# Optimization experiments

Measured on AMD Instinct MI355X. Metric: run time of the kernel, lower is better.

## Reference

```python
import jax, jax.numpy as jnp
import numpy as np

N, FIN = 4096, 128
HEADS = [8, 1]
FEATS = [64, 64]
NEG_SLOPE = 0.2
EDGE_P = 0.01  # edge density for the synthetic graph


def _init_w(key, shape, fan_in, fan_out):
    # VarianceScaling(1.0, 'fan_avg', 'uniform')
    limit = jnp.sqrt(3.0 / ((fan_in + fan_out) / 2.0))
    return jax.random.uniform(key, shape, jnp.float32, -limit, limit)


def setup_inputs() -> dict:
    key = jax.random.key(0)
    ks = jax.random.split(key, 12)
    x = jax.random.normal(ks[0], (N, FIN), jnp.float32)
    # additive connectivity mask: 0 on edges (incl. self-loops), -1e9 elsewhere
    adj = jax.random.bernoulli(ks[1], EDGE_P, (N, N))
    adj = adj | jnp.eye(N, dtype=bool)
    mask = jnp.where(adj, 0.0, -1e9).astype(jnp.float32)

    fin0, out0 = FIN, HEADS[0] * FEATS[0]
    fin1, out1 = out0, HEADS[1] * FEATS[1]
    W0 = _init_w(ks[2], (fin0, out0), fin0, out0)
    b0 = jnp.zeros((out0,), jnp.float32)
    a_src0 = _init_w(ks[3], (1, HEADS[0], FEATS[0]), 1, HEADS[0] * FEATS[0])
    a_tgt0 = _init_w(ks[4], (1, HEADS[0], FEATS[0]), 1, HEADS[0] * FEATS[0])
    W1 = _init_w(ks[5], (fin1, out1), fin1, out1)
    b1 = jnp.zeros((out1,), jnp.float32)
    a_src1 = _init_w(ks[6], (1, HEADS[1], FEATS[1]), 1, HEADS[1] * FEATS[1])
    a_tgt1 = _init_w(ks[7], (1, HEADS[1], FEATS[1]), 1, HEADS[1] * FEATS[1])
    return {
        "node_features": x, "connectivity_mask": mask,
        "W0": W0, "b0": b0, "a_src0": a_src0, "a_tgt0": a_tgt0,
        "W1": W1, "b1": b1, "a_src1": a_src1, "a_tgt1": a_tgt1,
    }


def _gat_layer(x, mask, W, b, a_src, a_tgt, num_heads, num_features):
    # (N, FIN) @ (FIN, H*F) -> (N, H, F)
    proj = (x @ W + b).reshape(-1, num_heads, num_features)
    s_src = jnp.sum(proj * a_src, axis=-1)  # (N, H)
    s_tgt = jnp.sum(proj * a_tgt, axis=-1)  # (N, H)
    # (H, N, 1) + (H, 1, N) -> (H, N, N)
    scores = s_src.T[:, :, None] + s_tgt.T[:, None, :]
    scores = jax.nn.leaky_relu(scores, negative_slope=NEG_SLOPE)
    att = jax.nn.softmax(scores + mask[None, :, :], axis=-1)  # (H, N, N)
    out = jnp.einsum('hnm,mhf->nhf', att, proj)  # (N, H, F)
    return out.reshape(-1, num_heads * num_features)


def reference(node_features, connectivity_mask, W0, b0, a_src0, a_tgt0,
              W1, b1, a_src1, a_tgt1):
    h = _gat_layer(node_features, connectivity_mask, W0, b0, a_src0, a_tgt0,
                   HEADS[0], FEATS[0])
    h = _gat_layer(h, connectivity_mask, W1, b1, a_src1, a_tgt1,
                   HEADS[1], FEATS[1])
    return h  # (N, HEADS[1]*FEATS[1])
```

## Files before the change

kernel.cpp:

```cpp
#include <hip/hip_runtime.h>
#include <hip/hip_bf16.h>

#define NNODES 4096
#define CAP 256


__global__ __launch_bounds__(256) void phase1_kernel(
    const float* __restrict__ mask, int* __restrict__ deg, int* __restrict__ cols,
    const float* __restrict__ x, const float* __restrict__ W0,
    const float* __restrict__ b0, const float* __restrict__ a_src0,
    const float* __restrict__ a_tgt0, float* __restrict__ proj0,
    float* __restrict__ ssrc0, float* __restrict__ stgt0) {
  __shared__ float smem[32 * 36 + 32 * 64];
  const int t = threadIdx.x;
  if (blockIdx.x >= 1024) {
    const int n = blockIdx.x - 1024;
    const int lane = t & 63, wid = t >> 6;
    int* wsum = (int*)smem;
    const float4* row = (const float4*)(mask + (size_t)n * NNODES);
    float4 v[4];
    int cnt = 0;
#pragma unroll
    for (int j = 0; j < 4; ++j) {
      v[j] = row[t + 256 * j];
      cnt += (v[j].x == 0.0f) + (v[j].y == 0.0f) + (v[j].z == 0.0f) +
             (v[j].w == 0.0f);
    }
    int xs = cnt;
#pragma unroll
    for (int o = 1; o < 64; o <<= 1) {
      int y = __shfl_up(xs, o);
      if (lane >= o) xs += y;
    }
    if (lane == 63) wsum[wid] = xs;
    __syncthreads();
    int base = 0;
    for (int w = 0; w < wid; ++w) base += wsum[w];
    int off = base + xs - cnt;
    if (t == 0) {
      int total = wsum[0] + wsum[1] + wsum[2] + wsum[3];
      deg[n] = total < CAP ? total : CAP;
    }
    int* dst = cols + (size_t)n * CAP;
#pragma unroll
    for (int j = 0; j < 4; ++j) {
      const int c0 = (t + 256 * j) * 4;
      float fv[4] = {v[j].x, v[j].y, v[j].z, v[j].w};
#pragma unroll
      for (int k = 0; k < 4; ++k) {
        if (fv[k] == 0.0f) {
          if (off < CAP) dst[off] = c0 + k;
          ++off;
        }
      }
    }
  } else {
    float(*As)[36] = (float(*)[36])smem;
    float(*Ws)[64] = (float(*)[64])(smem + 32 * 36);
    const int bx = blockIdx.x;
    const int brow = (bx & 127) * 32;
    const int head = bx >> 7;
    const int bcol = head * 64;
    const int tx = t & 15, ty = t >> 4;
    const int ar = t >> 3, ak = (t & 7) * 4;
    float acc[2][4] = {};
    for (int c = 0; c < 4; ++c) {
      const int k0 = c * 32;
      *(float4*)&As[ar][ak] =
          *(const float4*)&x[(size_t)(brow + ar) * 128 + k0 + ak];
#pragma unroll
      for (int q = 0; q < 2; ++q) {
        int i = t + q * 256;
        int k = i >> 4, c4 = (i & 15) * 4;
        *(float4*)&Ws[k][c4] =
            *(const float4*)&W0[(size_t)(k0 + k) * 512 + bcol + c4];
      }
      __syncthreads();
#pragma unroll 2
      for (int kk = 0; kk < 32; kk += 4) {
        float4 a0 = *(const float4*)&As[ty * 2 + 0][kk];
        float4 a1 = *(const float4*)&As[ty * 2 + 1][kk];
#pragma unroll
        for (int j = 0; j < 4; ++j) {
          float4 w = *(const float4*)&Ws[kk + j][tx * 4];
          float av0 = ((const float*)&a0)[j];
          float av1 = ((const float*)&a1)[j];
          acc[0][0] = fmaf(av0, w.x, acc[0][0]);
          acc[0][1] = fmaf(av0, w.y, acc[0][1]);
          acc[0][2] = fmaf(av0, w.z, acc[0][2]);
          acc[0][3] = fmaf(av0, w.w, acc[0][3]);
          acc[1][0] = fmaf(av1, w.x, acc[1][0]);
          acc[1][1] = fmaf(av1, w.y, acc[1][1]);
          acc[1][2] = fmaf(av1, w.z, acc[1][2]);
          acc[1][3] = fmaf(av1, w.w, acc[1][3]);
        }
      }
      __syncthreads();
    }
    const float4 bv = *(const float4*)&b0[bcol + tx * 4];
    const float4 as = *(const float4*)&a_src0[head * 64 + tx * 4];
    const float4 at = *(const float4*)&a_tgt0[head * 64 + tx * 4];
#pragma unroll
    for (int r = 0; r < 2; ++r) {
      float4 o;
      o.x = acc[r][0] + bv.x; o.y = acc[r][1] + bv.y;
      o.z = acc[r][2] + bv.z; o.w = acc[r][3] + bv.w;
      const size_t node = brow + ty * 2 + r;
      *(float4*)&proj0[node * 512 + bcol + tx * 4] = o;
      float ps = o.x * as.x + o.y * as.y + o.z * as.z + o.w * as.w;
      float pt = o.x * at.x + o.y * at.y + o.z * at.z + o.w * at.w;
#pragma unroll
      for (int m = 8; m; m >>= 1) {
        ps += __shfl_xor(ps, m);
        pt += __shfl_xor(pt, m);
      }
      if (tx == 0) {
        ssrc0[node * 8 + head] = ps;
        stgt0[node * 8 + head] = pt;
      }
    }
  }
}

__global__ __launch_bounds__(128) void attn8h_kernel(
    const float* __restrict__ proj0, const float* __restrict__ ssrc0,
    const float* __restrict__ stgt0, const int* __restrict__ deg,
    const int* __restrict__ cols, float* __restrict__ h0) {
  const int b = blockIdx.x;
  const int fh = (b & 7) >> 2;
  const int n = ((b >> 3) << 2) + (b & 3);
  const int t = threadIdx.x;
  const int lane = t & 63, wid = t >> 6;
  __shared__ int sm_[CAP];
  __shared__ float sw[CAP * 5];
  __shared__ float sinv[4];
  __shared__ float4 buf[64];
  const int d = deg[n];
  for (int i = t; i < d; i += 128) sm_[i] = cols[(size_t)n * CAP + i];
  __syncthreads();
  const int hbase = fh * 4;
  for (int i = t; i < d * 4; i += 128) {
    const int e = i >> 2, h = i & 3;
    float s = ssrc0[n * 8 + hbase + h] + stgt0[sm_[e] * 8 + hbase + h];
    sw[e * 5 + h] = s >= 0.f ? s : 0.2f * s;
  }
  __syncthreads();
  for (int h = wid; h < 4; h += 2) {
    float mx = -1e30f;
    for (int e = lane; e < d; e += 64) mx = fmaxf(mx, sw[e * 5 + h]);
#pragma unroll
    for (int o = 32; o; o >>= 1) mx = fmaxf(mx, __shfl_xor(mx, o));
    float sum = 0.f;
    for (int e = lane; e < d; e += 64) {
      float w = __expf(sw[e * 5 + h] - mx);
      sw[e * 5 + h] = w;
      sum += w;
    }
#pragma unroll
    for (int o = 32; o; o >>= 1) sum += __shfl_xor(sum, o);
    if (lane == 0) sinv[h] = 1.0f / sum;
  }
  __syncthreads();
  const int f4l = t & 63, grp = t >> 6;
  const int hl = f4l >> 4;
  float4 acc = make_float4(0.f, 0.f, 0.f, 0.f);
  for (int e = grp; e < d; e += 2) {
    const float w = sw[e * 5 + hl];
    const float4 pv =
        *(const float4*)&proj0[(size_t)sm_[e] * 512 + fh * 256 + f4l * 4];
    acc.x = fmaf(w, pv.x, acc.x);
    acc.y = fmaf(w, pv.y, acc.y);
    acc.z = fmaf(w, pv.z, acc.z);
    acc.w = fmaf(w, pv.w, acc.w);
  }
  if (grp == 1) buf[f4l] = acc;
  __syncthreads();
  if (grp == 0) {
    const float4 o2 = buf[f4l];
    const float s = sinv[hl];
    float4 o;
    o.x = (acc.x + o2.x) * s;
    o.y = (acc.y + o2.y) * s;
    o.z = (acc.z + o2.z) * s;
    o.w = (acc.w + o2.w) * s;
    *(float4*)&h0[(size_t)n * 512 + fh * 256 + f4l * 4] = o;
  }
}

__global__ __launch_bounds__(256) void gemm32x64_v2(
    const float* __restrict__ A, int lda, const float* __restrict__ W, int ldw,
    float* __restrict__ C, int ldc) {
  __shared__ float As[32][36];
  __shared__ float Ws[32][64];
  const int t = threadIdx.x;
  const int brow = blockIdx.x * 32;
  const int bcol = blockIdx.y * 64;
  const int k0base = blockIdx.z * 128;
  C += (size_t)blockIdx.z * gridDim.x * 32 * ldc;
  const int tx = t & 15, ty = t >> 4;
  const int ar = t >> 3, ak = (t & 7) * 4;
  float acc[2][4] = {};
  for (int c = 0; c < 4; ++c) {
    const int k0 = k0base + c * 32;
    *(float4*)&As[ar][ak] = *(const float4*)&A[(size_t)(brow + ar) * lda + k0 + ak];
#pragma unroll
    for (int q = 0; q < 2; ++q) {
      int i = t + q * 256;
      int k = i >> 4, c4 = (i & 15) * 4;
      *(float4*)&Ws[k][c4] = *(const float4*)&W[(size_t)(k0 + k) * ldw + bcol + c4];
    }
    __syncthreads();
#pragma unroll 2
    for (int kk = 0; kk < 32; kk += 4) {
      float4 a0 = *(const float4*)&As[ty * 2 + 0][kk];
      float4 a1 = *(const float4*)&As[ty * 2 + 1][kk];
#pragma unroll
      for (int j = 0; j < 4; ++j) {
        float4 w = *(const float4*)&Ws[kk + j][tx * 4];
        float av0 = ((const float*)&a0)[j];
        float av1 = ((const float*)&a1)[j];
        acc[0][0] = fmaf(av0, w.x, acc[0][0]);
        acc[0][1] = fmaf(av0, w.y, acc[0][1]);
        acc[0][2] = fmaf(av0, w.z, acc[0][2]);
        acc[0][3] = fmaf(av0, w.w, acc[0][3]);
        acc[1][0] = fmaf(av1, w.x, acc[1][0]);
        acc[1][1] = fmaf(av1, w.y, acc[1][1]);
        acc[1][2] = fmaf(av1, w.z, acc[1][2]);
        acc[1][3] = fmaf(av1, w.w, acc[1][3]);
      }
    }
    __syncthreads();
  }
#pragma unroll
  for (int r = 0; r < 2; ++r) {
    float4 o;
    o.x = acc[r][0]; o.y = acc[r][1]; o.z = acc[r][2]; o.w = acc[r][3];
    *(float4*)&C[(size_t)(brow + ty * 2 + r) * ldc + bcol + tx * 4] = o;
  }
}

__global__ __launch_bounds__(256) void reduce_scores1_kernel(
    const float* __restrict__ part, const float* __restrict__ bias,
    const float* __restrict__ a_src1, const float* __restrict__ a_tgt1,
    float* __restrict__ proj1, float* __restrict__ ssrc1,
    float* __restrict__ stgt1) {
  const int i = blockIdx.x * 256 + threadIdx.x;
  const float4* p = (const float4*)part;
  float4 a = p[i], b = p[i + 65536], c = p[i + 131072], d = p[i + 196608];
  const int f4 = i & 15;
  const float4 bb = *(const float4*)&bias[f4 * 4];
  float4 r;
  r.x = a.x + b.x + c.x + d.x + bb.x;
  r.y = a.y + b.y + c.y + d.y + bb.y;
  r.z = a.z + b.z + c.z + d.z + bb.z;
  r.w = a.w + b.w + c.w + d.w + bb.w;
  ((float4*)proj1)[i] = r;
  const float4 as = *(const float4*)&a_src1[f4 * 4];
  const float4 at = *(const float4*)&a_tgt1[f4 * 4];
  float ps = r.x * as.x + r.y * as.y + r.z * as.z + r.w * as.w;
  float pt = r.x * at.x + r.y * at.y + r.z * at.z + r.w * at.w;
#pragma unroll
  for (int m = 8; m; m >>= 1) {
    ps += __shfl_xor(ps, m);
    pt += __shfl_xor(pt, m);
  }
  if (f4 == 0) {
    const int node = i >> 4;
    ssrc1[node] = ps;
    stgt1[node] = pt;
  }
}

__global__ void attn1_kernel(
    const float* __restrict__ proj, const float* __restrict__ s_src,
    const float* __restrict__ s_tgt, const int* __restrict__ deg,
    const int* __restrict__ cols, float* __restrict__ out) {
  const int n = blockIdx.x;
  const int tid = threadIdx.x;
  __shared__ int sm_[CAP];
  __shared__ float sw[CAP];
  const int d = deg[n];
  for (int i = tid; i < d; i += 64) sm_[i] = cols[(size_t)n * CAP + i];
  __syncthreads();
  const float ssn = s_src[n];
  for (int i = tid; i < d; i += 64) {
    float s = ssn + s_tgt[sm_[i]];
    sw[i] = s >= 0.f ? s : 0.2f * s;
  }
  __syncthreads();
  float mx = -1e30f;
  for (int e = tid; e < d; e += 64) mx = fmaxf(mx, sw[e]);
#pragma unroll
  for (int o = 32; o; o >>= 1) mx = fmaxf(mx, __shfl_xor(mx, o));
  float sum = 0.f;
  for (int e = tid; e < d; e += 64) {
    float w = __expf(sw[e] - mx);
    sw[e] = w;
    sum += w;
  }
#pragma unroll
  for (int o = 32; o; o >>= 1) sum += __shfl_xor(sum, o);
  const float sinv = 1.0f / sum;
  __syncthreads();
  const int f4 = tid & 15, grp = tid >> 4;
  float4 acc = make_float4(0.f, 0.f, 0.f, 0.f);
  for (int e = grp; e < d; e += 4) {
    const float w = sw[e];
    const float4 pv = *(const float4*)&proj[(size_t)sm_[e] * 64 + f4 * 4];
    acc.x = fmaf(w, pv.x, acc.x);
    acc.y = fmaf(w, pv.y, acc.y);
    acc.z = fmaf(w, pv.z, acc.z);
    acc.w = fmaf(w, pv.w, acc.w);
  }
#pragma unroll
  for (int o = 16; o <= 32; o <<= 1) {
    acc.x += __shfl_xor(acc.x, o);
    acc.y += __shfl_xor(acc.y, o);
    acc.z += __shfl_xor(acc.z, o);
    acc.w += __shfl_xor(acc.w, o);
  }
  if (grp == 0) {
    acc.x *= sinv; acc.y *= sinv; acc.z *= sinv; acc.w *= sinv;
    *(float4*)&out[(size_t)n * 64 + f4 * 4] = acc;
  }
}

extern "C" void kernel_launch(void* const* d_in, const int* in_sizes, int n_in,
                              void* d_out, int out_size, void* d_ws, size_t ws_size,
                              hipStream_t stream) {
  const float* x      = (const float*)d_in[0];
  const float* mask   = (const float*)d_in[1];
  const float* W0     = (const float*)d_in[2];
  const float* b0     = (const float*)d_in[3];
  const float* a_src0 = (const float*)d_in[4];
  const float* a_tgt0 = (const float*)d_in[5];
  const float* W1     = (const float*)d_in[6];
  const float* b1     = (const float*)d_in[7];
  const float* a_src1 = (const float*)d_in[8];
  const float* a_tgt1 = (const float*)d_in[9];
  float* out = (float*)d_out;

  float* ws    = (float*)d_ws;
  float* proj0 = ws;
  float* h0    = proj0 + NNODES * 512;
  float* proj1 = h0 + NNODES * 512;
  float* ssrc0 = proj1 + NNODES * 64;
  float* stgt0 = ssrc0 + NNODES * 8;
  float* ssrc1 = stgt0 + NNODES * 8;
  float* stgt1 = ssrc1 + NNODES;
  int* deg  = (int*)(stgt1 + NNODES);
  int* cols = deg + NNODES;
  float* part = proj0;

  phase1_kernel<<<NNODES + 1024, 256, 0, stream>>>(
      mask, deg, cols, x, W0, b0, a_src0, a_tgt0, proj0, ssrc0, stgt0);
  attn8h_kernel<<<NNODES * 2, 128, 0, stream>>>(proj0, ssrc0, stgt0, deg, cols, h0);
  gemm32x64_v2<<<dim3(NNODES / 32, 1, 4), 256, 0, stream>>>(
      h0, 512, W1, 64, part, 64);
  reduce_scores1_kernel<<<256, 256, 0, stream>>>(part, b1, a_src1, a_tgt1,
                                                 proj1, ssrc1, stgt1);
  attn1_kernel<<<NNODES, 64, 0, stream>>>(proj1, ssrc1, stgt1, deg, cols, out);
}
```

Baseline: 69.38 us.

## Fold layer-1 weight into per-head projections before layer-0 aggregation

Uses linearity of the attention-weighted sum to multiply each head's projection tile by its slice of W1 inside the first GEMM kernel. The aggregation kernel then gathers the pre-transformed per-head 64-wide vectors, pre-normalizes the weights, reduces across heads with shuffles and writes two partial sums instead of the full 512-wide h0. This removes the separate layer-1 GEMM launch and the write and read of h0, and halves the partial-sum reduction. The cost is an extra small GEMM per phase1 block and a different floating-point summation order.

```diff
diff --git a/kernel.cpp b/kernel.cpp
--- a/kernel.cpp
+++ b/kernel.cpp
@@ -9,9 +9,10 @@
     const float* __restrict__ mask, int* __restrict__ deg, int* __restrict__ cols,
     const float* __restrict__ x, const float* __restrict__ W0,
     const float* __restrict__ b0, const float* __restrict__ a_src0,
-    const float* __restrict__ a_tgt0, float* __restrict__ proj0,
-    float* __restrict__ ssrc0, float* __restrict__ stgt0) {
-  __shared__ float smem[32 * 36 + 32 * 64];
+    const float* __restrict__ a_tgt0, const float* __restrict__ W1,
+    float* __restrict__ Ph, float* __restrict__ ssrc0,
+    float* __restrict__ stgt0) {
+  __shared__ float smem[6144];
   const int t = threadIdx.x;
   if (blockIdx.x >= 1024) {
     const int n = blockIdx.x - 1024;
@@ -56,7 +57,7 @@
     }
   } else {
     float(*As)[36] = (float(*)[36])smem;
-    float(*Ws)[64] = (float(*)[64])(smem + 32 * 36);
+    float(*Ws)[64] = (float(*)[64])(smem + 1152);
     const int bx = blockIdx.x;
     const int brow = (bx & 127) * 32;
     const int head = bx >> 7;
@@ -97,6 +98,8 @@
       }
       __syncthreads();
     }
+    float(*tile)[64] = (float(*)[64])smem;
+    float(*W1s)[64] = (float(*)[64])(smem + 2048);
     const float4 bv = *(const float4*)&b0[bcol + tx * 4];
     const float4 as = *(const float4*)&a_src0[head * 64 + tx * 4];
     const float4 at = *(const float4*)&a_tgt0[head * 64 + tx * 4];
@@ -105,8 +108,8 @@
       float4 o;
       o.x = acc[r][0] + bv.x; o.y = acc[r][1] + bv.y;
       o.z = acc[r][2] + bv.z; o.w = acc[r][3] + bv.w;
-      const size_t node = brow + ty * 2 + r;
-      *(float4*)&proj0[node * 512 + bcol + tx * 4] = o;
+      const int rowl = ty * 2 + r;
+      *(float4*)&tile[rowl][tx * 4] = o;
       float ps = o.x * as.x + o.y * as.y + o.z * as.z + o.w * as.w;
       float pt = o.x * at.x + o.y * at.y + o.z * at.z + o.w * at.w;
 #pragma unroll
@@ -115,17 +118,45 @@
         pt += __shfl_xor(pt, m);
       }
       if (tx == 0) {
+        const size_t node = brow + rowl;
         ssrc0[node * 8 + head] = ps;
         stgt0[node * 8 + head] = pt;
       }
     }
-  }
-}
-
-__global__ __launch_bounds__(128) void attn8h_kernel(
-    const float* __restrict__ proj0, const float* __restrict__ ssrc0,
+    for (int i = t; i < 1024; i += 256) {
+      const int k = i >> 4, c4 = (i & 15) * 4;
+      *(float4*)&W1s[k][c4] =
+          *(const float4*)&W1[(size_t)(head * 64 + k) * 64 + c4];
+    }
+    __syncthreads();
+    float acc2[2][4] = {};
+#pragma unroll 4
+    for (int k = 0; k < 64; ++k) {
+      const float4 w4 = *(const float4*)&W1s[k][tx * 4];
+      const float a0 = tile[ty * 2 + 0][k];
+      const float a1 = tile[ty * 2 + 1][k];
+      acc2[0][0] = fmaf(a0, w4.x, acc2[0][0]);
+      acc2[0][1] = fmaf(a0, w4.y, acc2[0][1]);
+      acc2[0][2] = fmaf(a0, w4.z, acc2[0][2]);
+      acc2[0][3] = fmaf(a0, w4.w, acc2[0][3]);
+      acc2[1][0] = fmaf(a1, w4.x, acc2[1][0]);
+      acc2[1][1] = fmaf(a1, w4.y, acc2[1][1]);
+      acc2[1][2] = fmaf(a1, w4.z, acc2[1][2]);
+      acc2[1][3] = fmaf(a1, w4.w, acc2[1][3]);
+    }
+#pragma unroll
+    for (int r = 0; r < 2; ++r) {
+      float4 o;
+      o.x = acc2[r][0]; o.y = acc2[r][1]; o.z = acc2[r][2]; o.w = acc2[r][3];
+      *(float4*)&Ph[(size_t)(brow + ty * 2 + r) * 512 + head * 64 + tx * 4] = o;
+    }
+  }
+}
+
+__global__ __launch_bounds__(128) void attnP_kernel(
+    const float* __restrict__ Ph, const float* __restrict__ ssrc0,
     const float* __restrict__ stgt0, const int* __restrict__ deg,
-    const int* __restrict__ cols, float* __restrict__ h0) {
+    const int* __restrict__ cols, float* __restrict__ part) {
   const int b = blockIdx.x;
   const int fh = (b & 7) >> 2;
   const int n = ((b >> 3) << 2) + (b & 3);
@@ -134,7 +165,7 @@
   __shared__ int sm_[CAP];
   __shared__ float sw[CAP * 5];
   __shared__ float sinv[4];
-  __shared__ float4 buf[64];
+  __shared__ float4 buf[16];
   const int d = deg[n];
   for (int i = t; i < d; i += 128) sm_[i] = cols[(size_t)n * CAP + i];
   __syncthreads();
@@ -161,99 +192,56 @@
     if (lane == 0) sinv[h] = 1.0f / sum;
   }
   __syncthreads();
-  const int f4l = t & 63, grp = t >> 6;
-  const int hl = f4l >> 4;
+  for (int i = t; i < d * 4; i += 128) {
+    const int e = i >> 2, h = i & 3;
+    sw[e * 5 + h] *= sinv[h];
+  }
+  __syncthreads();
+  const int grp = t >> 6;
+  const int hl = lane >> 4;
   float4 acc = make_float4(0.f, 0.f, 0.f, 0.f);
   for (int e = grp; e < d; e += 2) {
     const float w = sw[e * 5 + hl];
     const float4 pv =
-        *(const float4*)&proj0[(size_t)sm_[e] * 512 + fh * 256 + f4l * 4];
+        *(const float4*)&Ph[(size_t)sm_[e] * 512 + fh * 256 + lane * 4];
     acc.x = fmaf(w, pv.x, acc.x);
     acc.y = fmaf(w, pv.y, acc.y);
     acc.z = fmaf(w, pv.z, acc.z);
     acc.w = fmaf(w, pv.w, acc.w);
   }
-  if (grp == 1) buf[f4l] = acc;
-  __syncthreads();
-  if (grp == 0) {
-    const float4 o2 = buf[f4l];
-    const float s = sinv[hl];
+#pragma unroll
+  for (int o = 16; o <= 32; o <<= 1) {
+    acc.x += __shfl_xor(acc.x, o);
+    acc.y += __shfl_xor(acc.y, o);
+    acc.z += __shfl_xor(acc.z, o);
+    acc.w += __shfl_xor(acc.w, o);
+  }
+  if (grp == 1 && lane < 16) buf[lane] = acc;
+  __syncthreads();
+  if (grp == 0 && lane < 16) {
+    const float4 o2 = buf[lane];
     float4 o;
-    o.x = (acc.x + o2.x) * s;
-    o.y = (acc.y + o2.y) * s;
-    o.z = (acc.z + o2.z) * s;
-    o.w = (acc.w + o2.w) * s;
-    *(float4*)&h0[(size_t)n * 512 + fh * 256 + f4l * 4] = o;
-  }
-}
-
-__global__ __launch_bounds__(256) void gemm32x64_v2(
-    const float* __restrict__ A, int lda, const float* __restrict__ W, int ldw,
-    float* __restrict__ C, int ldc) {
-  __shared__ float As[32][36];
-  __shared__ float Ws[32][64];
-  const int t = threadIdx.x;
-  const int brow = blockIdx.x * 32;
-  const int bcol = blockIdx.y * 64;
-  const int k0base = blockIdx.z * 128;
-  C += (size_t)blockIdx.z * gridDim.x * 32 * ldc;
-  const int tx = t & 15, ty = t >> 4;
-  const int ar = t >> 3, ak = (t & 7) * 4;
-  float acc[2][4] = {};
-  for (int c = 0; c < 4; ++c) {
-    const int k0 = k0base + c * 32;
-    *(float4*)&As[ar][ak] = *(const float4*)&A[(size_t)(brow + ar) * lda + k0 + ak];
-#pragma unroll
-    for (int q = 0; q < 2; ++q) {
-      int i = t + q * 256;
-      int k = i >> 4, c4 = (i & 15) * 4;
-      *(float4*)&Ws[k][c4] = *(const float4*)&W[(size_t)(k0 + k) * ldw + bcol + c4];
-    }
-    __syncthreads();
-#pragma unroll 2
-    for (int kk = 0; kk < 32; kk += 4) {
-      float4 a0 = *(const float4*)&As[ty * 2 + 0][kk];
-      float4 a1 = *(const float4*)&As[ty * 2 + 1][kk];
-#pragma unroll
-      for (int j = 0; j < 4; ++j) {
-        float4 w = *(const float4*)&Ws[kk + j][tx * 4];
-        float av0 = ((const float*)&a0)[j];
-        float av1 = ((const float*)&a1)[j];
-        acc[0][0] = fmaf(av0, w.x, acc[0][0]);
-        acc[0][1] = fmaf(av0, w.y, acc[0][1]);
-        acc[0][2] = fmaf(av0, w.z, acc[0][2]);
-        acc[0][3] = fmaf(av0, w.w, acc[0][3]);
-        acc[1][0] = fmaf(av1, w.x, acc[1][0]);
-        acc[1][1] = fmaf(av1, w.y, acc[1][1]);
-        acc[1][2] = fmaf(av1, w.z, acc[1][2]);
-        acc[1][3] = fmaf(av1, w.w, acc[1][3]);
-      }
-    }
-    __syncthreads();
-  }
-#pragma unroll
-  for (int r = 0; r < 2; ++r) {
-    float4 o;
-    o.x = acc[r][0]; o.y = acc[r][1]; o.z = acc[r][2]; o.w = acc[r][3];
-    *(float4*)&C[(size_t)(brow + ty * 2 + r) * ldc + bcol + tx * 4] = o;
-  }
-}
-
-__global__ __launch_bounds__(256) void reduce_scores1_kernel(
+    o.x = acc.x + o2.x; o.y = acc.y + o2.y;
+    o.z = acc.z + o2.z; o.w = acc.w + o2.w;
+    *(float4*)&part[(size_t)fh * (NNODES * 64) + (size_t)n * 64 + lane * 4] = o;
+  }
+}
+
+__global__ __launch_bounds__(256) void finalize_scores1_kernel(
     const float* __restrict__ part, const float* __restrict__ bias,
     const float* __restrict__ a_src1, const float* __restrict__ a_tgt1,
     float* __restrict__ proj1, float* __restrict__ ssrc1,
     float* __restrict__ stgt1) {
   const int i = blockIdx.x * 256 + threadIdx.x;
   const float4* p = (const float4*)part;
-  float4 a = p[i], b = p[i + 65536], c = p[i + 131072], d = p[i + 196608];
+  float4 a = p[i], b = p[i + 65536];
   const int f4 = i & 15;
   const float4 bb = *(const float4*)&bias[f4 * 4];
   float4 r;
-  r.x = a.x + b.x + c.x + d.x + bb.x;
-  r.y = a.y + b.y + c.y + d.y + bb.y;
-  r.z = a.z + b.z + c.z + d.z + bb.z;
-  r.w = a.w + b.w + c.w + d.w + bb.w;
+  r.x = a.x + b.x + bb.x;
+  r.y = a.y + b.y + bb.y;
+  r.z = a.z + b.z + bb.z;
+  r.w = a.w + b.w + bb.w;
   ((float4*)proj1)[i] = r;
   const float4 as = *(const float4*)&a_src1[f4 * 4];
   const float4 at = *(const float4*)&a_tgt1[f4 * 4];
@@ -341,23 +329,20 @@
   float* out = (float*)d_out;
 
   float* ws    = (float*)d_ws;
-  float* proj0 = ws;
-  float* h0    = proj0 + NNODES * 512;
-  float* proj1 = h0 + NNODES * 512;
+  float* Ph    = ws;
+  float* part  = Ph + NNODES * 512;
+  float* proj1 = part + 2 * NNODES * 64;
   float* ssrc0 = proj1 + NNODES * 64;
   float* stgt0 = ssrc0 + NNODES * 8;
   float* ssrc1 = stgt0 + NNODES * 8;
   float* stgt1 = ssrc1 + NNODES;
   int* deg  = (int*)(stgt1 + NNODES);
   int* cols = deg + NNODES;
-  float* part = proj0;
 
   phase1_kernel<<<NNODES + 1024, 256, 0, stream>>>(
-      mask, deg, cols, x, W0, b0, a_src0, a_tgt0, proj0, ssrc0, stgt0);
-  attn8h_kernel<<<NNODES * 2, 128, 0, stream>>>(proj0, ssrc0, stgt0, deg, cols, h0);
-  gemm32x64_v2<<<dim3(NNODES / 32, 1, 4), 256, 0, stream>>>(
-      h0, 512, W1, 64, part, 64);
-  reduce_scores1_kernel<<<256, 256, 0, stream>>>(part, b1, a_src1, a_tgt1,
-                                                 proj1, ssrc1, stgt1);
+      mask, deg, cols, x, W0, b0, a_src0, a_tgt0, W1, Ph, ssrc0, stgt0);
+  attnP_kernel<<<NNODES * 2, 128, 0, stream>>>(Ph, ssrc0, stgt0, deg, cols, part);
+  finalize_scores1_kernel<<<256, 256, 0, stream>>>(part, b1, a_src1, a_tgt1,
+                                                   proj1, ssrc1, stgt1);
   attn1_kernel<<<NNODES, 64, 0, stream>>>(proj1, ssrc1, stgt1, deg, cols, out);
 }
```

Result: faster. 64.29 us (-7.3%).
